# Optimization experiments

Measured on AMD Instinct MI355X. Metric: run time of the kernel, lower is better.

Reference implementation:

```python
import jax, jax.numpy as jnp
import numpy as np

D_MODEL = 1024
N_HEADS = 16
B, T = 4, 2048


def setup_inputs() -> dict:
    key = jax.random.key(0)
    ks = jax.random.split(key, 5)
    s_in = 1.0 / np.sqrt(D_MODEL)
    x = jax.random.normal(ks[0], (B, T, D_MODEL), dtype=jnp.float32)
    W_qkv = jax.random.uniform(ks[1], (D_MODEL, 3 * D_MODEL), jnp.float32, -s_in, s_in)
    b_qkv = jax.random.uniform(ks[2], (3 * D_MODEL,), jnp.float32, -s_in, s_in)
    W_proj = jax.random.uniform(ks[3], (D_MODEL, D_MODEL), jnp.float32, -s_in, s_in)
    b_proj = jax.random.uniform(ks[4], (D_MODEL,), jnp.float32, -s_in, s_in)
    return {"x": x, "W_qkv": W_qkv, "b_qkv": b_qkv, "W_proj": W_proj, "b_proj": b_proj}


def reference(x, W_qkv, b_qkv, W_proj, b_proj):
    b, t, c = x.shape
    hd = c // N_HEADS  # head dim
    qkv = x @ W_qkv + b_qkv                      # [B,T,3C]
    q, k, v = jnp.split(qkv, 3, axis=2)
    # [B,T,C] -> [B,H,T,hd]
    def heads(z):
        return z.reshape(b, t, N_HEADS, hd).transpose(0, 2, 1, 3)
    q, k, v = heads(q), heads(k), heads(v)
    att = jnp.einsum('bhqd,bhkd->bhqk', q, k) * (1.0 / np.sqrt(hd))
    causal = jnp.tril(jnp.ones((t, t), dtype=bool))
    att = jnp.where(causal, att, -jnp.inf)
    att = jax.nn.softmax(att, axis=-1)
    y = jnp.einsum('bhqk,bhkd->bhqd', att, v)    # [B,H,T,hd]
    y = y.transpose(0, 2, 1, 3).reshape(b, t, c)
    return y @ W_proj + b_proj
```

## Files before the change

### kernel.cpp

```cpp
#include <hip/hip_runtime.h>
#include <hip/hip_bf16.h>

typedef __attribute__((ext_vector_type(4))) float f32x4;
typedef __attribute__((ext_vector_type(8))) short s16x8;
typedef __attribute__((ext_vector_type(4))) short s16x4;

#define D_MODEL 1024
#define NH 16
#define HD 64
#define BB 4
#define TT 2048
#define MROWS (BB * TT)
#define QSCALE 0.18033688011112042f

#define MFMA16(a, b, c) __builtin_amdgcn_mfma_f32_16x16x32_bf16(a, b, c, 0, 0, 0)

#if __has_builtin(__builtin_amdgcn_mfma_f32_16x16x16_bf16)
#define PVMFMA(a, b, c) __builtin_amdgcn_mfma_f32_16x16x16_bf16(a, b, c, 0, 0, 0)
#elif __has_builtin(__builtin_amdgcn_mfma_f32_16x16x16bf16_1k)
#define PVMFMA(a, b, c) __builtin_amdgcn_mfma_f32_16x16x16bf16_1k(a, b, c, 0, 0, 0)
#else
static __device__ __forceinline__ f32x4 pv_mfma_asm(s16x4 a, s16x4 b, f32x4 c) {
  asm volatile("v_mfma_f32_16x16x16_bf16 %0, %1, %2, %0\n\ts_nop 7\n\ts_nop 7"
               : "+v"(c)
               : "v"(a), "v"(b));
  return c;
}
#define PVMFMA(a, b, c) pv_mfma_asm(a, b, c)
#endif

#define GLL16(g, l)                                                                   \
  __builtin_amdgcn_global_load_lds((const __attribute__((address_space(1))) void*)(g), \
                                   (__attribute__((address_space(3))) void*)(l), 16, 0, 0)

static __device__ __forceinline__ unsigned short f2bf(float f) {
  unsigned int u = __float_as_uint(f);
  u += 0x7fff + ((u >> 16) & 1);
  return (unsigned short)(u >> 16);
}

__global__ void k_convert(const float* __restrict__ src, short* __restrict__ dst, int n4) {
  int i = blockIdx.x * blockDim.x + threadIdx.x;
  if (i >= n4) return;
  f32x4 v = reinterpret_cast<const f32x4*>(src)[i];
  s16x4 o;
#pragma unroll
  for (int r = 0; r < 4; r++) o[r] = (short)f2bf(v[r]);
  reinterpret_cast<s16x4*>(dst)[i] = o;
}

__global__ void k_transpose(const float* __restrict__ src, short* __restrict__ dst, int K, int N) {
  __shared__ float tile[32][33];
  int n0 = blockIdx.x * 32, k0 = blockIdx.y * 32;
  int tx = threadIdx.x, ty = threadIdx.y;
#pragma unroll
  for (int i = 0; i < 4; i++) tile[ty + i * 8][tx] = src[(size_t)(k0 + ty + i * 8) * N + n0 + tx];
  __syncthreads();
#pragma unroll
  for (int i = 0; i < 4; i++)
    dst[(size_t)(n0 + ty + i * 8) * K + k0 + tx] = (short)f2bf(tile[tx][ty + i * 8]);
}

template <int MODE>
__global__ __launch_bounds__(256, 2) void k_gemm(
    const short* __restrict__ A, const short* __restrict__ Bt, const float* __restrict__ bias,
    int K, int N, short* __restrict__ outQ, short* __restrict__ outK, short* __restrict__ outV,
    float* __restrict__ outF) {
  __shared__ __align__(16) short lds_a[2][128 * 32];
  __shared__ __align__(16) short lds_b[2][128 * 32];
  const int tid = threadIdx.x;
  const int m0 = blockIdx.y * 128, n0 = blockIdx.x * 128;
  const int w = tid >> 6, lane = tid & 63;
  const int wm = (w >> 1) * 64, wn = (w & 1) * 64;
  const int lr = lane & 15, lg = lane >> 4;

  const short* aG = A + (size_t)(m0 + w * 32 + (lane >> 2)) * K + (lane & 3) * 8;
  const short* bG = Bt + (size_t)(n0 + w * 32 + (lane >> 2)) * K + (lane & 3) * 8;
  short* aL = &lds_a[0][(w * 32) * 32];
  short* bL = &lds_b[0][(w * 32) * 32];

#define GSTAGE(bi, kt)                                                \
  {                                                                   \
    GLL16(aG + (kt), aL + (bi) * (128 * 32));                         \
    GLL16(aG + (size_t)16 * K + (kt), aL + (bi) * (128 * 32) + 512);  \
    GLL16(bG + (kt), bL + (bi) * (128 * 32));                         \
    GLL16(bG + (size_t)16 * K + (kt), bL + (bi) * (128 * 32) + 512);  \
  }

  f32x4 acc[4][4] = {};
  const int NT = K / 32;
  GSTAGE(0, 0);
  __syncthreads();
  for (int t = 0; t < NT; ++t) {
    const int cur = t & 1;
    if (t + 1 < NT) GSTAGE(cur ^ 1, (t + 1) * 32);
    s16x8 af[4], bfg[4];
#pragma unroll
    for (int i = 0; i < 4; i++) af[i] = *(const s16x8*)&lds_a[cur][(wm + i * 16 + lr) * 32 + lg * 8];
#pragma unroll
    for (int j = 0; j < 4; j++) bfg[j] = *(const s16x8*)&lds_b[cur][(wn + j * 16 + lr) * 32 + lg * 8];
#pragma unroll
    for (int i = 0; i < 4; i++) {
#pragma unroll
      for (int j = 0; j < 4; j++) acc[i][j] = MFMA16(af[i], bfg[j], acc[i][j]);
    }
    __syncthreads();
  }
#undef GSTAGE

#pragma unroll
  for (int j = 0; j < 4; j++) {
    const int ng = n0 + wn + j * 16 + lr;
    const float bv = bias[ng];
#pragma unroll
    for (int i = 0; i < 4; i++) {
      const int mg = m0 + wm + i * 16 + 4 * lg;
      if (MODE == 0) {
        const int sec = ng >> 10, c = ng & 1023, h = c >> 6, d = c & 63;
        const int b = mg >> 11, t = mg & 2047;
        const int bh = b * NH + h;
        if (sec == 2) {
          s16x4 pk;
#pragma unroll
          for (int r = 0; r < 4; r++) pk[r] = (short)f2bf(acc[i][j][r] + bv);
          *(s16x4*)&outV[((size_t)bh * HD + d) * TT + t] = pk;
        } else {
          short* dst = (sec == 0) ? outQ : outK;
          const float sc = (sec == 0) ? QSCALE : 1.0f;
#pragma unroll
          for (int r = 0; r < 4; r++)
            dst[((size_t)bh * TT + t + r) * HD + d] = (short)f2bf((acc[i][j][r] + bv) * sc);
        }
      } else {
#pragma unroll
        for (int r = 0; r < 4; r++) outF[(size_t)(mg + r) * N + ng] = acc[i][j][r] + bv;
      }
    }
  }
}

__global__ __launch_bounds__(256, 4) void k_attn(const short* __restrict__ Q,
                                                 const short* __restrict__ Kb,
                                                 const short* __restrict__ Vt,
                                                 short* __restrict__ Y) {
  __shared__ __align__(16) short kls[2][64 * 64];
  __shared__ __align__(16) short vls[2][64 * 64];
  const int tid = threadIdx.x, w = tid >> 6, lane = tid & 63;
  const int lr = lane & 15, lg = lane >> 4;
  const int bh = blockIdx.y;
  const int b = bh >> 4, h = bh & 15;
  const short* Qh = Q + (size_t)bh * TT * HD;
  const short* Kh = Kb + (size_t)bh * TT * HD;
  const short* Vh = Vt + (size_t)bh * HD * TT;
  const int srow = lane >> 3;
  const int scol = ((lane & 7) ^ srow) * 8;
  const int r7 = lr & 7;

#define STAGE(bi, kv0)                                                   \
  {                                                                      \
    const short* ks_ = Kh + (size_t)((kv0) + w * 16 + srow) * HD + scol; \
    GLL16(ks_, &kls[bi][(w * 16) * 64]);                                 \
    GLL16(ks_ + 8 * HD, &kls[bi][(w * 16 + 8) * 64]);                    \
    const short* vs_ = Vh + (size_t)(w * 16 + srow) * TT + (kv0) + scol; \
    GLL16(vs_, &vls[bi][(w * 16) * 64]);                                 \
    GLL16(vs_ + 8 * TT, &vls[bi][(w * 16 + 8) * 64]);                    \
  }

#pragma unroll
  for (int ph = 0; ph < 2; ph++) {
    const int panel = ph ? (31 - blockIdx.x) : blockIdx.x;
    const int q0w = panel * 64 + w * 16;
    s16x8 qf[2];
#pragma unroll
    for (int kc = 0; kc < 2; kc++)
      qf[kc] = *(const s16x8*)&Qh[(q0w + lr) * HD + kc * 32 + lg * 8];

    float lacc = 0.f;
    f32x4 oacc[4] = {};

    const int nt = panel + 1;
    STAGE(0, 0);
    __syncthreads();
    for (int t = 0; t < nt; ++t) {
      const int cur = t & 1;
      if (t + 1 < nt) STAGE(cur ^ 1, (t + 1) * 64);
      const int kv0 = t * 64;
      s16x8 kf[4][2];
#pragma unroll
      for (int jk = 0; jk < 4; jk++)
#pragma unroll
        for (int kc = 0; kc < 2; kc++)
          kf[jk][kc] = *(const s16x8*)&kls[cur][(jk * 16 + lr) * 64 + ((kc * 4 + lg) ^ r7) * 8];
      f32x4 s[4] = {};
#pragma unroll
      for (int kc = 0; kc < 2; kc++)
#pragma unroll
        for (int jk = 0; jk < 4; jk++) s[jk] = MFMA16(kf[jk][kc], qf[kc], s[jk]);

      const bool diag = (kv0 + 63 > q0w);
      const int qg = q0w + lr;
      s16x4 pf16[4];
#pragma unroll
      for (int jk = 0; jk < 4; jk++) {
#pragma unroll
        for (int r = 0; r < 4; r++) {
          float p = exp2f(s[jk][r]);
          if (diag) {
            const int kvg = kv0 + jk * 16 + 4 * lg + r;
            p = (kvg <= qg) ? p : 0.f;
          }
          lacc += p;
          pf16[jk][r] = (short)((__float_as_uint(p) + 0x8000) >> 16);
        }
      }
#pragma unroll
      for (int jk = 0; jk < 4; jk++) {
        s16x4 vreg[4];
#pragma unroll
        for (int jd = 0; jd < 4; jd++)
          vreg[jd] = *(const s16x4*)&vls[cur][(jd * 16 + lr) * 64 +
                                              ((2 * jk + (lg >> 1)) ^ r7) * 8 + (lg & 1) * 4];
#pragma unroll
        for (int jd = 0; jd < 4; jd++) oacc[jd] = PVMFMA(vreg[jd], pf16[jk], oacc[jd]);
      }
      __syncthreads();
    }
    float lrow = lacc;
    lrow += __shfl_xor(lrow, 16);
    lrow += __shfl_xor(lrow, 32);
    const float inv = 1.0f / lrow;
    const int trow = q0w + lr;
#pragma unroll
    for (int jd = 0; jd < 4; jd++) {
      s16x4 pk;
#pragma unroll
      for (int r = 0; r < 4; r++) pk[r] = (short)f2bf(oacc[jd][r] * inv);
      *(s16x4*)&Y[((size_t)(b * TT + trow)) * D_MODEL + h * HD + jd * 16 + 4 * lg] = pk;
    }
  }
#undef STAGE
}

extern "C" void kernel_launch(void* const* d_in, const int* in_sizes, int n_in,
                              void* d_out, int out_size, void* d_ws, size_t ws_size,
                              hipStream_t stream) {
  const float* x = (const float*)d_in[0];
  const float* Wqkv = (const float*)d_in[1];
  const float* bqkv = (const float*)d_in[2];
  const float* Wproj = (const float*)d_in[3];
  const float* bproj = (const float*)d_in[4];
  float* out = (float*)d_out;

  char* ws = (char*)d_ws;
  short* Xb = (short*)ws;
  short* Wqkvt = (short*)(ws + (16u << 20));
  short* Wprojt = (short*)(ws + (22u << 20));
  short* Qb = (short*)(ws + (24u << 20));
  short* Kb = (short*)(ws + (40u << 20));
  short* Vtb = (short*)(ws + (56u << 20));
  short* Yb = Xb;

  k_convert<<<dim3(MROWS * D_MODEL / 4 / 256), 256, 0, stream>>>(x, Xb, MROWS * D_MODEL / 4);
  k_transpose<<<dim3(3 * D_MODEL / 32, D_MODEL / 32), dim3(32, 8), 0, stream>>>(
      Wqkv, Wqkvt, D_MODEL, 3 * D_MODEL);
  k_transpose<<<dim3(D_MODEL / 32, D_MODEL / 32), dim3(32, 8), 0, stream>>>(
      Wproj, Wprojt, D_MODEL, D_MODEL);
  k_gemm<0><<<dim3(3 * D_MODEL / 128, MROWS / 128), 256, 0, stream>>>(
      Xb, Wqkvt, bqkv, D_MODEL, 3 * D_MODEL, Qb, Kb, Vtb, nullptr);
  k_attn<<<dim3(16, BB * NH), 256, 0, stream>>>(Qb, Kb, Vtb, Yb);
  k_gemm<1><<<dim3(D_MODEL / 128, MROWS / 128), 256, 0, stream>>>(
      Yb, Wprojt, bproj, D_MODEL, D_MODEL, nullptr, nullptr, nullptr, out);
}
```

Before: 285.0 us.

## Triple-buffer GEMM LDS pipeline and compute softmax row sums via MFMA

The GEMM main loop moves from double to triple buffering of the A/B LDS tiles. It prefetches two k-steps ahead, uses explicit vmcnt waits with raw barriers, and raises launch bounds to 3 blocks per CU, so global-load latency is better hidden. In attention, the per-lane scalar accumulation of softmax denominators plus cross-lane shuffles is replaced by an extra PV MFMA against a ones vector. This sums the bf16-rounded P values on the matrix unit. The cost is more LDS per GEMM block, possible register pressure from the occupancy target, and one additional MFMA per key tile.

Result: no change. 281.4 us (-1.3%).

```diff
diff --git a/kernel.cpp b/kernel.cpp
--- a/kernel.cpp
+++ b/kernel.cpp
@@ -62,12 +62,12 @@
 }
 
 template <int MODE>
-__global__ __launch_bounds__(256, 2) void k_gemm(
+__global__ __launch_bounds__(256, 3) void k_gemm(
     const short* __restrict__ A, const short* __restrict__ Bt, const float* __restrict__ bias,
     int K, int N, short* __restrict__ outQ, short* __restrict__ outK, short* __restrict__ outV,
     float* __restrict__ outF) {
-  __shared__ __align__(16) short lds_a[2][128 * 32];
-  __shared__ __align__(16) short lds_b[2][128 * 32];
+  __shared__ __align__(16) short lds_a[3][128 * 32];
+  __shared__ __align__(16) short lds_b[3][128 * 32];
   const int tid = threadIdx.x;
   const int m0 = blockIdx.y * 128, n0 = blockIdx.x * 128;
   const int w = tid >> 6, lane = tid & 63;
@@ -76,35 +76,48 @@
 
   const short* aG = A + (size_t)(m0 + w * 32 + (lane >> 2)) * K + (lane & 3) * 8;
   const short* bG = Bt + (size_t)(n0 + w * 32 + (lane >> 2)) * K + (lane & 3) * 8;
-  short* aL = &lds_a[0][(w * 32) * 32];
-  short* bL = &lds_b[0][(w * 32) * 32];
-
-#define GSTAGE(bi, kt)                                                \
-  {                                                                   \
-    GLL16(aG + (kt), aL + (bi) * (128 * 32));                         \
-    GLL16(aG + (size_t)16 * K + (kt), aL + (bi) * (128 * 32) + 512);  \
-    GLL16(bG + (kt), bL + (bi) * (128 * 32));                         \
-    GLL16(bG + (size_t)16 * K + (kt), bL + (bi) * (128 * 32) + 512);  \
+
+#define GSTAGE(bi, kt)                                        \
+  {                                                           \
+    GLL16(aG + (kt), &lds_a[bi][(w * 32) * 32]);              \
+    GLL16(aG + (size_t)16 * K + (kt), &lds_a[bi][(w * 32 + 16) * 32]); \
+    GLL16(bG + (kt), &lds_b[bi][(w * 32) * 32]);              \
+    GLL16(bG + (size_t)16 * K + (kt), &lds_b[bi][(w * 32 + 16) * 32]); \
   }
 
   f32x4 acc[4][4] = {};
   const int NT = K / 32;
   GSTAGE(0, 0);
-  __syncthreads();
+  GSTAGE(1, 32);
+  asm volatile("s_waitcnt vmcnt(4)" ::: "memory");
+  __builtin_amdgcn_s_barrier();
+  __builtin_amdgcn_sched_barrier(0);
+  int cur = 0, nx2 = 2;
   for (int t = 0; t < NT; ++t) {
-    const int cur = t & 1;
-    if (t + 1 < NT) GSTAGE(cur ^ 1, (t + 1) * 32);
+    if (t + 2 < NT) GSTAGE(nx2, (t + 2) * 32);
     s16x8 af[4], bfg[4];
 #pragma unroll
-    for (int i = 0; i < 4; i++) af[i] = *(const s16x8*)&lds_a[cur][(wm + i * 16 + lr) * 32 + lg * 8];
-#pragma unroll
-    for (int j = 0; j < 4; j++) bfg[j] = *(const s16x8*)&lds_b[cur][(wn + j * 16 + lr) * 32 + lg * 8];
+    for (int i = 0; i < 4; i++)
+      af[i] = *(const s16x8*)&lds_a[cur][(wm + i * 16 + lr) * 32 + lg * 8];
+#pragma unroll
+    for (int j = 0; j < 4; j++)
+      bfg[j] = *(const s16x8*)&lds_b[cur][(wn + j * 16 + lr) * 32 + lg * 8];
 #pragma unroll
     for (int i = 0; i < 4; i++) {
 #pragma unroll
       for (int j = 0; j < 4; j++) acc[i][j] = MFMA16(af[i], bfg[j], acc[i][j]);
     }
-    __syncthreads();
+    if (t + 2 < NT) {
+      asm volatile("s_waitcnt vmcnt(4) lgkmcnt(0)" ::: "memory");
+      __builtin_amdgcn_s_barrier();
+      __builtin_amdgcn_sched_barrier(0);
+    } else if (t + 1 < NT) {
+      asm volatile("s_waitcnt vmcnt(0) lgkmcnt(0)" ::: "memory");
+      __builtin_amdgcn_s_barrier();
+      __builtin_amdgcn_sched_barrier(0);
+    }
+    cur = (cur == 2) ? 0 : cur + 1;
+    nx2 = (nx2 == 2) ? 0 : nx2 + 1;
   }
 #undef GSTAGE
 
@@ -155,6 +168,7 @@
   const int srow = lane >> 3;
   const int scol = ((lane & 7) ^ srow) * 8;
   const int r7 = lr & 7;
+  const s16x4 vone = {(short)0x3F80, (short)0x3F80, (short)0x3F80, (short)0x3F80};
 
 #define STAGE(bi, kv0)                                                   \
   {                                                                      \
@@ -175,7 +189,7 @@
     for (int kc = 0; kc < 2; kc++)
       qf[kc] = *(const s16x8*)&Qh[(q0w + lr) * HD + kc * 32 + lg * 8];
 
-    float lacc = 0.f;
+    f32x4 sacc = {0.f, 0.f, 0.f, 0.f};
     f32x4 oacc[4] = {};
 
     const int nt = panel + 1;
@@ -209,7 +223,6 @@
             const int kvg = kv0 + jk * 16 + 4 * lg + r;
             p = (kvg <= qg) ? p : 0.f;
           }
-          lacc += p;
           pf16[jk][r] = (short)((__float_as_uint(p) + 0x8000) >> 16);
         }
       }
@@ -220,15 +233,13 @@
         for (int jd = 0; jd < 4; jd++)
           vreg[jd] = *(const s16x4*)&vls[cur][(jd * 16 + lr) * 64 +
                                               ((2 * jk + (lg >> 1)) ^ r7) * 8 + (lg & 1) * 4];
+        sacc = PVMFMA(vone, pf16[jk], sacc);
 #pragma unroll
         for (int jd = 0; jd < 4; jd++) oacc[jd] = PVMFMA(vreg[jd], pf16[jk], oacc[jd]);
       }
       __syncthreads();
     }
-    float lrow = lacc;
-    lrow += __shfl_xor(lrow, 16);
-    lrow += __shfl_xor(lrow, 32);
-    const float inv = 1.0f / lrow;
+    const float inv = 1.0f / sacc[0];
     const int trow = q0w + lr;
 #pragma unroll
     for (int jd = 0; jd < 4; jd++) {
```
